# Kernel tuning notes

Measured on AMD Instinct MI355X. Metric: run time of the kernel, lower is better.

Reference implementation:

```python
import jax, jax.numpy as jnp
import numpy as np


def conv1x1(x, w, b):
    # 1x1 conv: x [B,C,H,W], w [O,C], b [O]
    return jnp.einsum('bchw,oc->bohw', x, w) + b[None, :, None, None]


def _propagate(x, w_red, b_red, w_u, b_u, w_lam, b_lam, w_wt, b_wt, direction):
    transposed = direction in ('lr', 'rl')
    reverse = direction in ('bt', 'rl')
    prop_dim = 2 if direction in ('tb', 'bt') else 3
    reduced = conv1x1(x, w_red, b_red)
    u = conv1x1(reduced, w_u, b_u)
    lam = conv1x1(reduced, w_lam, b_lam)
    pre = conv1x1(reduced, w_wt, b_wt)
    if transposed:
        x, lam, pre, u = (t.swapaxes(-1, -2) for t in (x, lam, pre, u))
    if reverse:
        x, lam, pre, u = (jnp.flip(t, axis=prop_dim) for t in (x, lam, pre, u))
    S = x.shape[prop_dim]  # square input: H == W == S
    # sigmoid + channel-normalize the 3 tridiagonal band weights
    wn = jax.nn.sigmoid(pre)
    wn = wn / jnp.maximum(wn.sum(axis=1, keepdims=True), 1e-6)
    # In the original, hidden is broadcast identically over the row's j entries,
    # so (hidden[...,None]*tridiag_row).sum(-1) == hidden * rowsum(tridiag_row).
    # Row i has band entries at j = i-1, i, i+1 (where in range), all valued wn[:,k,...,i].
    wk = wn if prop_dim == 2 else wn.swapaxes(2, 3)  # [B,3,m,i]
    idx = jnp.arange(S)
    valid = jnp.stack([idx >= 1, jnp.ones((S,), bool), idx <= S - 2]).astype(wk.dtype)  # [3,S]
    R = (wk * valid[None, :, None, :]).sum(axis=1)  # [B,m,i] tridiagonal row-sums
    Rseq = jnp.moveaxis(R, -1, 0)  # [S,B,m]
    step_axis = 2 if transposed else 3  # axis of x indexed per step (as in original)
    Xseq = jnp.moveaxis(x, step_axis, 0)       # [S,B,C,m]
    Lseq = jnp.moveaxis(lam, 5 - step_axis, 0)  # lambda indexed on the other spatial axis

    def step(h, inp):
        r, xi, li = inp
        h = h * r[:, None, :] + li * xi
        return h, h

    h0 = jnp.zeros_like(Xseq[0])  # [B,C,m]
    _, ys = jax.lax.scan(step, h0, (Rseq, Xseq, Lseq))  # ys [S,B,C,m]
    out = jnp.moveaxis(ys, 0, 2 if transposed else 3)
    if reverse:
        out = jnp.flip(out, axis=prop_dim)
    out = out * u
    if transposed:
        out = out.swapaxes(-1, -2)
    return out


def _forward(x, w_red, b_red, w_u, b_u, w_lam, b_lam, w_wt, b_wt, w_merge, b_merge):
    outs = [_propagate(x, w_red, b_red, w_u, b_u, w_lam, b_lam, w_wt, b_wt, d)
            for d in ('tb', 'bt', 'lr', 'rl')]
    concat = jnp.concatenate(outs, axis=1)  # [B,4C,H,W]
    # NOTE: the original also computes a softmax-merged tensor that is discarded;
    # the returned output is merge(concat) only.
    return conv1x1(concat, w_merge, b_merge)


def setup_inputs() -> dict:
    key = jax.random.key(0)
    ks = jax.random.split(key, 11)
    B, C, S = 8, 256, 64
    Cr = C // 4
    f32 = jnp.float32
    x = jax.random.normal(ks[0], (B, C, S, S), f32)
    w_red = jax.random.normal(ks[1], (Cr, C), f32) * C ** -0.5
    b_red = jax.random.normal(ks[2], (Cr,), f32) * 0.01
    w_u = jax.random.normal(ks[3], (C, Cr), f32) * Cr ** -0.5
    b_u = jax.random.normal(ks[4], (C,), f32) * 0.01
    w_lam = jax.random.normal(ks[5], (C, Cr), f32) * Cr ** -0.5
    b_lam = jax.random.normal(ks[6], (C,), f32) * 0.01
    w_wt = jax.random.normal(ks[7], (3, Cr), f32) * Cr ** -0.5
    b_wt = jax.random.normal(ks[8], (3,), f32) * 0.01
    w_merge = jax.random.normal(ks[9], (C, 4 * C), f32) * (4 * C) ** -0.5
    b_merge = jax.random.normal(ks[10], (C,), f32) * 0.01
    return {"x": x, "w_red": w_red, "b_red": b_red, "w_u": w_u, "b_u": b_u,
            "w_lam": w_lam, "b_lam": b_lam, "w_wt": w_wt, "b_wt": b_wt,
            "w_merge": w_merge, "b_merge": b_merge}


def reference(x, w_red, b_red, w_u, b_u, w_lam, b_lam, w_wt, b_wt, w_merge, b_merge):
    return _forward(x, w_red, b_red, w_u, b_u, w_lam, b_lam, w_wt, b_wt, w_merge, b_merge)
```

## Files before the change

### kernel.cpp

```cpp
#include <hip/hip_runtime.h>


typedef __attribute__((ext_vector_type(8))) short short8b;
typedef __attribute__((ext_vector_type(4))) float f32x4;
typedef __attribute__((ext_vector_type(2))) unsigned int uint2v;
typedef __attribute__((ext_vector_type(4))) unsigned int uint4v;

__device__ __forceinline__ unsigned short bf16_rne(float v) {
  unsigned u = __float_as_uint(v);
  unsigned r = u + 0x7FFF + ((u >> 16) & 1);
  return (unsigned short)(r >> 16);
}
__device__ __forceinline__ float bf16_f(unsigned short h) {
  return __uint_as_float((unsigned)h << 16);
}

#define TR_READ8(q0,q1,q2,q3,q4,q5,q6,q7,va0,va1,va2,va3)                      \
  asm volatile("ds_read_b64_tr_b16 %0, %8\n\t"                                 \
               "ds_read_b64_tr_b16 %1, %8 offset:128\n\t"                      \
               "ds_read_b64_tr_b16 %2, %9\n\t"                                 \
               "ds_read_b64_tr_b16 %3, %9 offset:128\n\t"                      \
               "ds_read_b64_tr_b16 %4, %10\n\t"                                \
               "ds_read_b64_tr_b16 %5, %10 offset:128\n\t"                     \
               "ds_read_b64_tr_b16 %6, %11\n\t"                                \
               "ds_read_b64_tr_b16 %7, %11 offset:128\n\t"                     \
               "s_waitcnt lgkmcnt(0)"                                          \
               : "=&v"(q0), "=&v"(q1), "=&v"(q2), "=&v"(q3),                   \
                 "=&v"(q4), "=&v"(q5), "=&v"(q6), "=&v"(q7)                    \
               : "v"(va0), "v"(va1), "v"(va2), "v"(va3))

__global__ __launch_bounds__(256) void k_red(const float* __restrict__ x,
    const float* __restrict__ w_red, const float* __restrict__ b_red,
    const float* __restrict__ w_wt, const float* __restrict__ b_wt,
    const float* __restrict__ w_u, const float* __restrict__ w_lam,
    const float* __restrict__ w_merge,
    unsigned short* __restrict__ red2, float* __restrict__ R0,
    unsigned short* __restrict__ wu2, unsigned short* __restrict__ wlam2,
    unsigned short* __restrict__ W2T) {
  const int t = threadIdx.x;
  if (blockIdx.x >= 64) {
    int e = (blockIdx.x - 64) * 8 + blockIdx.y;
#pragma unroll
    for (int i = 0; i < 10; i++) {
      int flat = e * 2560 + i * 256 + t;
      if (flat < 16384) {
        wu2[flat] = bf16_rne(w_u[flat]);
      } else if (flat < 32768) {
        wlam2[flat - 16384] = bf16_rne(w_lam[flat - 16384]);
      } else {
        int mm = flat - 32768;
        int o = mm >> 9, cc = mm & 511;
        float v = w_merge[o * 1024 + cc] + w_merge[o * 1024 + cc + 512];
        W2T[mm] = bf16_rne(v);
      }
    }
    return;
  }
  __shared__ float xs[64][68];
  __shared__ float ws[64][68];
  int b = blockIdx.y;
  int px0 = blockIdx.x * 64;
  int pxg = t & 15, mg = t >> 4;
  const int tm = t & 63, tcg = t >> 6;
  float acc[4][4] = {};
  for (int ch = 0; ch < 4; ch++) {
    int c0 = ch * 64;
#pragma unroll
    for (int i = 0; i < 4; i++) {
      int idx4 = i * 256 + t;
      int kk = idx4 >> 4, j4 = idx4 & 15;
      *(float4*)&xs[kk][j4 * 4] =
          *(const float4*)(x + ((size_t)b << 20) + ((size_t)kk + c0 << 12) + px0 + j4 * 4);
    }
#pragma unroll
    for (int s = 0; s < 4; s++) {
      int cc = tcg * 16 + s * 4;
      float4 v = *(const float4*)(w_red + tm * 256 + c0 + cc);
      ws[cc + 0][tm] = v.x; ws[cc + 1][tm] = v.y;
      ws[cc + 2][tm] = v.z; ws[cc + 3][tm] = v.w;
    }
    __syncthreads();
#pragma unroll 8
    for (int kk = 0; kk < 64; kk++) {
      float4 a = *(float4*)&xs[kk][pxg * 4];
      float4 w = *(float4*)&ws[kk][mg * 4];
      float aa[4] = {a.x, a.y, a.z, a.w}, wv[4] = {w.x, w.y, w.z, w.w};
#pragma unroll
      for (int j = 0; j < 4; j++)
#pragma unroll
        for (int i = 0; i < 4; i++) acc[j][i] = fmaf(wv[j], aa[i], acc[j][i]);
    }
    __syncthreads();
  }
#pragma unroll
  for (int j = 0; j < 4; j++) {
    int m = mg * 4 + j;
    float bv = b_red[m];
    float v0 = acc[j][0] + bv, v1 = acc[j][1] + bv, v2 = acc[j][2] + bv, v3 = acc[j][3] + bv;
    ushort4 uv = make_ushort4(bf16_rne(v0), bf16_rne(v1), bf16_rne(v2), bf16_rne(v3));
    *(ushort4*)(red2 + ((size_t)b << 18) + ((size_t)m << 12) + px0 + pxg * 4) = uv;
    float* d = &xs[m][pxg * 4];
    d[0] = v0; d[1] = v1; d[2] = v2; d[3] = v3;
  }
  __syncthreads();
  float* preS = &ws[0][0];
  if (t < 192) {
    int j = t >> 6, px = t & 63;
    float a = b_wt[j];
    for (int kk = 0; kk < 64; kk++) a = fmaf(w_wt[j * 64 + kk], xs[kk][px], a);
    preS[j * 64 + px] = a;
  }
  __syncthreads();
  if (t < 64) {
    float s0 = 1.f / (1.f + __expf(-preS[t]));
    float s1 = 1.f / (1.f + __expf(-preS[64 + t]));
    float s2 = 1.f / (1.f + __expf(-preS[128 + t]));
    int w = t;
    float num = s1 + (w >= 1 ? s0 : 0.f) + (w <= 62 ? s2 : 0.f);
    R0[((size_t)b << 12) + px0 + t] = num / fmaxf(s0 + s1 + s2, 1e-6f);
  }
}

__global__ __launch_bounds__(256) void k_ulam(const unsigned short* __restrict__ red2,
    const unsigned short* __restrict__ wu2, const float* __restrict__ b_u,
    const unsigned short* __restrict__ wlam2, const float* __restrict__ b_lam,
    unsigned short* __restrict__ u, unsigned short* __restrict__ lam) {
  __shared__ __align__(16) unsigned short WL[256 * 72];
  __shared__ __align__(16) unsigned short PL[4096];
  const int t = threadIdx.x;
  const int px0 = blockIdx.x * 64;
  const int b = blockIdx.y;
  const int mt = blockIdx.z;
  const unsigned short* Wsrc = (mt == 0) ? wu2 : wlam2;
  const float* bias = (mt == 0) ? b_u : b_lam;
  unsigned short* dst = (mt == 0) ? u : lam;
  const unsigned short* red2b = red2 + ((size_t)b << 18);
  const int lane = t & 63;
  const int ln15 = lane & 15, lg = lane >> 4;
  const int ow = (t >> 6) * 64;

#pragma unroll
  for (int i = 0; i < 8; i++) {
    int unit = i * 256 + t, wrow = unit >> 3, wp = unit & 7;
    *(short8b*)&WL[wrow * 72 + wp * 8] = *(const short8b*)(Wsrc + wrow * 64 + wp * 8);
  }
#pragma unroll
  for (int i = 0; i < 2; i++) {
    int unit = i * 256 + t, kk = unit >> 3, ap = unit & 7;
    int off = ((ap >> 1) << 10) + ((kk >> 2) << 6) + ((kk & 3) << 4) + (ap & 1) * 8;
    *(short8b*)&PL[off] = *(const short8b*)(red2b + (size_t)kk * 4096 + px0 + ap * 8);
  }
  __syncthreads();

  f32x4 acc[4][4];
#pragma unroll
  for (int i = 0; i < 4; i++)
#pragma unroll
    for (int j = 0; j < 4; j++) acc[i][j] = (f32x4){0.f, 0.f, 0.f, 0.f};

  const unsigned pbase = (unsigned)(size_t)(&PL[0]);
  const unsigned vab = pbase + (unsigned)(lg * 256 + ln15 * 8);
#pragma unroll
  for (int kstep = 0; kstep < 2; kstep++) {
    short8b am[4];
#pragma unroll
    for (int i = 0; i < 4; i++)
      am[i] = *(const short8b*)&WL[(ow + i * 16 + ln15) * 72 + kstep * 32 + lg * 8];
    unsigned va0 = vab + kstep * 1024;
    unsigned va1 = va0 + 2048, va2 = va0 + 4096, va3 = va0 + 6144;
    uint2v q0, q1, q2, q3, q4, q5, q6, q7;
    TR_READ8(q0, q1, q2, q3, q4, q5, q6, q7, va0, va1, va2, va3);
    __builtin_amdgcn_sched_barrier(0);
    uint4v bu[4] = {(uint4v){q0.x, q0.y, q1.x, q1.y}, (uint4v){q2.x, q2.y, q3.x, q3.y},
                    (uint4v){q4.x, q4.y, q5.x, q5.y}, (uint4v){q6.x, q6.y, q7.x, q7.y}};
#pragma unroll
    for (int i = 0; i < 4; i++)
#pragma unroll
      for (int j = 0; j < 4; j++)
        acc[i][j] = __builtin_amdgcn_mfma_f32_16x16x32_bf16(
            am[i], __builtin_bit_cast(short8b, bu[j]), acc[i][j], 0, 0, 0);
  }

#pragma unroll
  for (int i = 0; i < 4; i++) {
    int orow = ow + i * 16 + lg * 4;
    float bm[4];
#pragma unroll
    for (int r = 0; r < 4; r++) bm[r] = bias[orow + r];
#pragma unroll
    for (int j = 0; j < 4; j++) {
      int pxc = px0 + j * 16 + ln15;
#pragma unroll
      for (int r = 0; r < 4; r++)
        dst[((size_t)b << 20) + ((size_t)(orow + r) << 12) + pxc] =
            bf16_rne(acc[i][j][r] + bm[r]);
    }
  }
}

__global__ __launch_bounds__(256) void k_scan(const float* __restrict__ x,
    const unsigned short* __restrict__ lam, const unsigned short* __restrict__ u,
    const float* __restrict__ R0, unsigned short* __restrict__ P2,
    unsigned short* __restrict__ Q2) {
  __shared__ __align__(16) char smem[20224];
  float* lamS = (float*)smem;
  unsigned* outS = (unsigned*)smem;
  float* fixS = (float*)(smem + 16896);
  const int t = threadIdx.x;
  const int c = blockIdx.x;
  const int b = blockIdx.y;
  const size_t ibase = ((size_t)b << 20) + ((size_t)c << 12);

  {
    const unsigned short* lp = lam + ibase;
#pragma unroll
    for (int i = 0; i < 2; i++) {
      int unit = i * 256 + t;
      int row = unit >> 3, c8 = unit & 7;
      short8b v = *(const short8b*)(lp + row * 64 + c8 * 8);
      float* d = &lamS[row * 65 + c8 * 8];
#pragma unroll
      for (int j = 0; j < 8; j++) d[j] = bf16_f((unsigned short)v[j]);
    }
  }
  const int r = t & 63;
  const int qc = __builtin_amdgcn_readfirstlane(t >> 6);
  float xr[16], R[16];
  {
    const float* xp = x + ibase + (r << 6) + (qc << 4);
    const float* rp = R0 + ((size_t)b << 12) + (r << 6) + (qc << 4);
#pragma unroll
    for (int i = 0; i < 4; i++) {
      float4 v = *(const float4*)(xp + i * 4);
      xr[i * 4] = v.x; xr[i * 4 + 1] = v.y; xr[i * 4 + 2] = v.z; xr[i * 4 + 3] = v.w;
      float4 w = *(const float4*)(rp + i * 4);
      R[i * 4] = w.x; R[i * 4 + 1] = w.y; R[i * 4 + 2] = w.z; R[i * 4 + 3] = w.w;
    }
  }
  __syncthreads();
  float g1[16], g2[16];
  float A = 1.f, B1 = 0.f, B2 = 0.f;
#pragma unroll
  for (int j = 0; j < 16; j++) {
    int w = (qc << 4) + j;
    float l1 = lamS[w * 65 + r];
    float l2 = lamS[(63 - w) * 65 + (63 - r)];
    g1[j] = l1 * xr[j];
    g2[j] = l2 * xr[j];
    A *= R[j];
    B1 = fmaf(B1, R[j], g1[j]);
    B2 = fmaf(B2, R[j], g2[j]);
  }
  __syncthreads();
  fixS[r * 13 + qc * 3 + 0] = A;
  fixS[r * 13 + qc * 3 + 1] = B1;
  fixS[r * 13 + qc * 3 + 2] = B2;
  __syncthreads();
  float h1 = 0.f, h2 = 0.f;
  for (int p = 0; p < qc; p++) {
    float Ap  = fixS[r * 13 + p * 3 + 0];
    float Bp1 = fixS[r * 13 + p * 3 + 1];
    float Bp2 = fixS[r * 13 + p * 3 + 2];
    h1 = fmaf(h1, Ap, Bp1);
    h2 = fmaf(h2, Ap, Bp2);
  }
  float ur[16], fr[16];
  {
    const unsigned short* up = u + ibase + (r << 6) + (qc << 4);
    const unsigned short* fp = u + ibase + ((size_t)(63 - r) << 6) + (qc << 4);
    short8b u0 = *(const short8b*)(up);
    short8b u1 = *(const short8b*)(up + 8);
    short8b f0 = *(const short8b*)(fp);
    short8b f1 = *(const short8b*)(fp + 8);
#pragma unroll
    for (int j = 0; j < 8; j++) {
      ur[j] = bf16_f((unsigned short)u0[j]); ur[8 + j] = bf16_f((unsigned short)u1[j]);
      fr[j] = bf16_f((unsigned short)f0[j]); fr[8 + j] = bf16_f((unsigned short)f1[j]);
    }
  }
#pragma unroll
  for (int j2 = 0; j2 < 8; j2++) {
    int j = j2 * 2;
    h1 = fmaf(h1, R[j], g1[j]);         float p0 = h1 * ur[j];
    h2 = fmaf(h2, R[j], g2[j]);         float q0 = h2 * fr[j];
    h1 = fmaf(h1, R[j + 1], g1[j + 1]); float p1 = h1 * ur[j + 1];
    h2 = fmaf(h2, R[j + 1], g2[j + 1]); float q1 = h2 * fr[j + 1];
    int ob = r * 33 + (qc << 3) + j2;
    outS[ob]        = (unsigned)bf16_rne(p0) | ((unsigned)bf16_rne(p1) << 16);
    outS[2112 + ob] = (unsigned)bf16_rne(q0) | ((unsigned)bf16_rne(q1) << 16);
  }
  __syncthreads();
#pragma unroll
  for (int i = 0; i < 4; i++) {
    int flat4 = i * 256 + t;
    int s = flat4 >> 9;
    int rem = flat4 & 511;
    int row = rem >> 3, c8 = rem & 7;
    const unsigned* ls = &outS[s * 2112 + row * 33 + c8 * 4];
    uint4 v = make_uint4(ls[0], ls[1], ls[2], ls[3]);
    unsigned short* base = (s == 0) ? P2 : Q2;
    size_t off = ((size_t)(b * 256 + c)) * 4096 + row * 64 + c8 * 8;
    *(uint4*)(base + off) = v;
  }
}

__global__ __launch_bounds__(256) void k_merge(
    const unsigned short* __restrict__ P2, const unsigned short* __restrict__ Q2,
    const unsigned short* __restrict__ W2T, const float* __restrict__ b_merge,
    float* __restrict__ out) {
  __shared__ __align__(16) unsigned short WL[256 * 72];
  __shared__ __align__(16) unsigned short PL[4096];
  const int t = threadIdx.x;
  const int px0 = blockIdx.x * 64;
  const int b = blockIdx.y;
  const int lane = t & 63;
  const int ln15 = lane & 15, lg = lane >> 4;
  const int ow = (t >> 6) * 64;

  const unsigned short* P2b = P2 + (size_t)b * 256 * 4096;
  const unsigned short* Q2b = Q2 + (size_t)b * 256 * 4096;

  f32x4 acc[4][4];
#pragma unroll
  for (int i = 0; i < 4; i++)
#pragma unroll
    for (int j = 0; j < 4; j++) acc[i][j] = (f32x4){0.f, 0.f, 0.f, 0.f};

  short8b wreg[8], preg[2];
#pragma unroll
  for (int i = 0; i < 8; i++) {
    int unit = i * 256 + t, wrow = unit >> 3, wp = unit & 7;
    wreg[i] = *(const short8b*)(W2T + (size_t)wrow * 512 + wp * 8);
  }
#pragma unroll
  for (int i = 0; i < 2; i++) {
    int unit = i * 256 + t, kk = unit >> 3, ap = unit & 7;
    preg[i] = *(const short8b*)(P2b + (size_t)kk * 4096 + px0 + ap * 8);
  }

  const unsigned pbase = (unsigned)(size_t)(&PL[0]);
  const unsigned vab = pbase + (unsigned)(lg * 256 + ln15 * 8);

  for (int it = 0; it < 8; ++it) {
    __syncthreads();
#pragma unroll
    for (int i = 0; i < 8; i++) {
      int unit = i * 256 + t, wrow = unit >> 3, wp = unit & 7;
      *(short8b*)&WL[wrow * 72 + wp * 8] = wreg[i];
    }
#pragma unroll
    for (int i = 0; i < 2; i++) {
      int unit = i * 256 + t, kk = unit >> 3, ap = unit & 7;
      int off = ((ap >> 1) << 10) + ((kk >> 2) << 6) + ((kk & 3) << 4) + (ap & 1) * 8;
      *(short8b*)&PL[off] = preg[i];
    }
    __syncthreads();
    if (it < 7) {
      int nt = it + 1;
#pragma unroll
      for (int i = 0; i < 8; i++) {
        int unit = i * 256 + t, wrow = unit >> 3, wp = unit & 7;
        wreg[i] = *(const short8b*)(W2T + (size_t)wrow * 512 + nt * 64 + wp * 8);
      }
      const unsigned short* ps = (nt < 4) ? P2b : Q2b;
      int row0 = (nt & 3) * 64;
#pragma unroll
      for (int i = 0; i < 2; i++) {
        int unit = i * 256 + t, kk = unit >> 3, ap = unit & 7;
        preg[i] = *(const short8b*)(ps + (size_t)(row0 + kk) * 4096 + px0 + ap * 8);
      }
    }
#pragma unroll
    for (int kstep = 0; kstep < 2; kstep++) {
      short8b am[4];
#pragma unroll
      for (int i = 0; i < 4; i++)
        am[i] = *(const short8b*)&WL[(ow + i * 16 + ln15) * 72 + kstep * 32 + lg * 8];
      unsigned va0 = vab + kstep * 1024;
      unsigned va1 = va0 + 2048, va2 = va0 + 4096, va3 = va0 + 6144;
      uint2v q0, q1, q2, q3, q4, q5, q6, q7;
      TR_READ8(q0, q1, q2, q3, q4, q5, q6, q7, va0, va1, va2, va3);
      __builtin_amdgcn_sched_barrier(0);
      uint4v bu[4] = {(uint4v){q0.x, q0.y, q1.x, q1.y}, (uint4v){q2.x, q2.y, q3.x, q3.y},
                      (uint4v){q4.x, q4.y, q5.x, q5.y}, (uint4v){q6.x, q6.y, q7.x, q7.y}};
#pragma unroll
      for (int i = 0; i < 4; i++)
#pragma unroll
        for (int j = 0; j < 4; j++)
          acc[i][j] = __builtin_amdgcn_mfma_f32_16x16x32_bf16(
              am[i], __builtin_bit_cast(short8b, bu[j]), acc[i][j], 0, 0, 0);
    }
  }

#pragma unroll
  for (int i = 0; i < 4; i++) {
    int orow = ow + i * 16 + lg * 4;
    float bm[4];
#pragma unroll
    for (int r = 0; r < 4; r++) bm[r] = b_merge[orow + r];
#pragma unroll
    for (int j = 0; j < 4; j++) {
      int pxc = px0 + j * 16 + ln15;
      float* op = out + ((size_t)b << 20) + ((size_t)orow << 12) + pxc;
#pragma unroll
      for (int r = 0; r < 4; r++) op[(size_t)r << 12] = acc[i][j][r] + bm[r];
    }
  }
}

extern "C" void kernel_launch(void* const* d_in, const int* in_sizes, int n_in,
                              void* d_out, int out_size, void* d_ws, size_t ws_size,
                              hipStream_t stream) {
  const float* x       = (const float*)d_in[0];
  const float* w_red   = (const float*)d_in[1];
  const float* b_red   = (const float*)d_in[2];
  const float* w_u     = (const float*)d_in[3];
  const float* b_u     = (const float*)d_in[4];
  const float* w_lam   = (const float*)d_in[5];
  const float* b_lam   = (const float*)d_in[6];
  const float* w_wt    = (const float*)d_in[7];
  const float* b_wt    = (const float*)d_in[8];
  const float* w_merge = (const float*)d_in[9];
  const float* b_merge = (const float*)d_in[10];
  float* out = (float*)d_out;
  char* wsb = (char*)d_ws;

  unsigned short* red2  = (unsigned short*)(wsb);
  unsigned short* u     = (unsigned short*)(wsb + 4194304);
  unsigned short* lam   = (unsigned short*)(wsb + 20971520);
  float* R0             = (float*)(wsb + 37748736);
  unsigned short* wu2   = (unsigned short*)(wsb + 37879808);
  unsigned short* wlam2 = (unsigned short*)(wsb + 37912576);
  unsigned short* W2T   = (unsigned short*)(wsb + 37945344);
  unsigned short* P2    = (unsigned short*)(wsb + 38207488);
  unsigned short* Q2    = (unsigned short*)(wsb + 54984704);

  hipLaunchKernelGGL(k_red,   dim3(72, 8),    dim3(256), 0, stream, x, w_red, b_red,
                     w_wt, b_wt, w_u, w_lam, w_merge, red2, R0, wu2, wlam2, W2T);
  hipLaunchKernelGGL(k_ulam,  dim3(64, 8, 2), dim3(256), 0, stream, red2, wu2, b_u,
                     wlam2, b_lam, u, lam);
  hipLaunchKernelGGL(k_scan,  dim3(256, 8),   dim3(256), 0, stream, x, lam, u, R0, P2, Q2);
  hipLaunchKernelGGL(k_merge, dim3(64, 8),    dim3(256), 0, stream, P2, Q2, W2T, b_merge, out);
}
```

Measured before the change: 78.63 us.

## Use bf16 MFMA for channel-reduction conv with register-prefetched tiles

The reduction 1x1 conv in k_red moves from a scalar FP32 FMA loop to bf16 MFMA 16x16x32 instructions. Weights and activations are converted to bf16 in registers, staged in LDS (activations in a layout for transposed reads), and the next channel chunk is prefetched into registers while the current one is computed. This cuts ALU work and LDS traffic but lowers the precision of the reduced features to bf16 inputs. The red2 stores become scalar ushort writes instead of vectorized ones.

```diff
diff --git a/kernel.cpp b/kernel.cpp
--- a/kernel.cpp
+++ b/kernel.cpp
@@ -13,6 +13,16 @@
 }
 __device__ __forceinline__ float bf16_f(unsigned short h) {
   return __uint_as_float((unsigned)h << 16);
+}
+__device__ __forceinline__ short8b cvt8(const float* p) {
+  float4 a = *(const float4*)p;
+  float4 c = *(const float4*)(p + 4);
+  short8b r;
+  r[0] = (short)bf16_rne(a.x); r[1] = (short)bf16_rne(a.y);
+  r[2] = (short)bf16_rne(a.z); r[3] = (short)bf16_rne(a.w);
+  r[4] = (short)bf16_rne(c.x); r[5] = (short)bf16_rne(c.y);
+  r[6] = (short)bf16_rne(c.z); r[7] = (short)bf16_rne(c.w);
+  return r;
 }
 
 #define TR_READ8(q0,q1,q2,q3,q4,q5,q6,q7,va0,va1,va2,va3)                      \
@@ -57,53 +67,81 @@
     return;
   }
   __shared__ float xs[64][68];
-  __shared__ float ws[64][68];
-  int b = blockIdx.y;
-  int px0 = blockIdx.x * 64;
-  int pxg = t & 15, mg = t >> 4;
-  const int tm = t & 63, tcg = t >> 6;
-  float acc[4][4] = {};
-  for (int ch = 0; ch < 4; ch++) {
-    int c0 = ch * 64;
-#pragma unroll
-    for (int i = 0; i < 4; i++) {
-      int idx4 = i * 256 + t;
-      int kk = idx4 >> 4, j4 = idx4 & 15;
-      *(float4*)&xs[kk][j4 * 4] =
-          *(const float4*)(x + ((size_t)b << 20) + ((size_t)kk + c0 << 12) + px0 + j4 * 4);
-    }
-#pragma unroll
-    for (int s = 0; s < 4; s++) {
-      int cc = tcg * 16 + s * 4;
-      float4 v = *(const float4*)(w_red + tm * 256 + c0 + cc);
-      ws[cc + 0][tm] = v.x; ws[cc + 1][tm] = v.y;
-      ws[cc + 2][tm] = v.z; ws[cc + 3][tm] = v.w;
-    }
+  __shared__ __align__(16) unsigned short WL[64 * 72];
+  __shared__ __align__(16) unsigned short PL[4096];
+  const int b = blockIdx.y;
+  const int px0 = blockIdx.x * 64;
+  const int lane = t & 63;
+  const int ln15 = lane & 15, lg = lane >> 4;
+  const int wv = t >> 6;
+  const int wrow = t >> 3 & 63, wp8 = t & 7;
+
+  f32x4 acc[4];
+#pragma unroll
+  for (int j = 0; j < 4; j++) acc[j] = (f32x4){0.f, 0.f, 0.f, 0.f};
+
+  short8b wreg[2], xreg[2];
+#pragma unroll
+  for (int i = 0; i < 2; i++) {
+    int unit = i * 256 + t;
+    int wr = unit >> 3, wp = unit & 7;
+    wreg[i] = cvt8(w_red + wr * 256 + wp * 8);
+    xreg[i] = cvt8(x + ((size_t)b << 20) + ((size_t)wr << 12) + px0 + wp * 8);
+  }
+  const unsigned pbase = (unsigned)(size_t)(&PL[0]);
+  const unsigned vab = pbase + (unsigned)(lg * 256 + ln15 * 8);
+
+  for (int ch = 0; ch < 4; ++ch) {
     __syncthreads();
-#pragma unroll 8
-    for (int kk = 0; kk < 64; kk++) {
-      float4 a = *(float4*)&xs[kk][pxg * 4];
-      float4 w = *(float4*)&ws[kk][mg * 4];
-      float aa[4] = {a.x, a.y, a.z, a.w}, wv[4] = {w.x, w.y, w.z, w.w};
+#pragma unroll
+    for (int i = 0; i < 2; i++) {
+      int unit = i * 256 + t;
+      int kk = unit >> 3, ap = unit & 7;
+      *(short8b*)&WL[kk * 72 + ap * 8] = wreg[i];
+      int off = ((ap >> 1) << 10) + ((kk >> 2) << 6) + ((kk & 3) << 4) + (ap & 1) * 8;
+      *(short8b*)&PL[off] = xreg[i];
+    }
+    __syncthreads();
+    if (ch < 3) {
+      int c0 = (ch + 1) * 64;
+#pragma unroll
+      for (int i = 0; i < 2; i++) {
+        int unit = i * 256 + t;
+        int wr = unit >> 3, wp = unit & 7;
+        wreg[i] = cvt8(w_red + wr * 256 + c0 + wp * 8);
+        xreg[i] = cvt8(x + ((size_t)b << 20) + ((size_t)(c0 + wr) << 12) + px0 + wp * 8);
+      }
+    }
+#pragma unroll
+    for (int kstep = 0; kstep < 2; kstep++) {
+      short8b am = *(const short8b*)&WL[(wv * 16 + ln15) * 72 + kstep * 32 + lg * 8];
+      unsigned va0 = vab + kstep * 1024;
+      unsigned va1 = va0 + 2048, va2 = va0 + 4096, va3 = va0 + 6144;
+      uint2v q0, q1, q2, q3, q4, q5, q6, q7;
+      TR_READ8(q0, q1, q2, q3, q4, q5, q6, q7, va0, va1, va2, va3);
+      __builtin_amdgcn_sched_barrier(0);
+      uint4v bu[4] = {(uint4v){q0.x, q0.y, q1.x, q1.y}, (uint4v){q2.x, q2.y, q3.x, q3.y},
+                      (uint4v){q4.x, q4.y, q5.x, q5.y}, (uint4v){q6.x, q6.y, q7.x, q7.y}};
 #pragma unroll
       for (int j = 0; j < 4; j++)
-#pragma unroll
-        for (int i = 0; i < 4; i++) acc[j][i] = fmaf(wv[j], aa[i], acc[j][i]);
-    }
-    __syncthreads();
-  }
+        acc[j] = __builtin_amdgcn_mfma_f32_16x16x32_bf16(
+            am, __builtin_bit_cast(short8b, bu[j]), acc[j], 0, 0, 0);
+    }
+  }
+  __syncthreads();
 #pragma unroll
   for (int j = 0; j < 4; j++) {
-    int m = mg * 4 + j;
-    float bv = b_red[m];
-    float v0 = acc[j][0] + bv, v1 = acc[j][1] + bv, v2 = acc[j][2] + bv, v3 = acc[j][3] + bv;
-    ushort4 uv = make_ushort4(bf16_rne(v0), bf16_rne(v1), bf16_rne(v2), bf16_rne(v3));
-    *(ushort4*)(red2 + ((size_t)b << 18) + ((size_t)m << 12) + px0 + pxg * 4) = uv;
-    float* d = &xs[m][pxg * 4];
-    d[0] = v0; d[1] = v1; d[2] = v2; d[3] = v3;
-  }
-  __syncthreads();
-  float* preS = &ws[0][0];
+    int pxl = j * 16 + ln15;
+#pragma unroll
+    for (int r = 0; r < 4; r++) {
+      int m = wv * 16 + lg * 4 + r;
+      float v = acc[j][r] + b_red[m];
+      xs[m][pxl] = v;
+      red2[((size_t)b << 18) + ((size_t)m << 12) + px0 + pxl] = bf16_rne(v);
+    }
+  }
+  __syncthreads();
+  float* preS = (float*)&WL[0];
   if (t < 192) {
     int j = t >> 6, px = t & 63;
     float a = b_wt[j];
```

Measured after the change: 62.97 us. -19.9%, faster.
